# Optimization experiments

Hardware: AMD Instinct MI355X
Metric: run time of the kernel (lower is better)

## Reference

```python
import jax, jax.numpy as jnp
import numpy as np

C = 64   # in_planes
F = 40   # n_freq
T = 512  # n_frame
B = 16


def setup_inputs() -> dict:
    key = jax.random.key(0)
    kx, kq, kk, kv = jax.random.split(key, 4)
    x = jax.random.normal(kx, (B, C, F, T), dtype=jnp.float32)
    # 1x1 conv weights, no bias: [out_ch, in_ch]
    s = 1.0 / np.sqrt(C)
    Wq = jax.random.uniform(kq, (C, C), dtype=jnp.float32, minval=-s, maxval=s)
    Wk = jax.random.uniform(kk, (C, C), dtype=jnp.float32, minval=-s, maxval=s)
    Wv = jax.random.uniform(kv, (C, C), dtype=jnp.float32, minval=-s, maxval=s)
    return {"x": x, "Wq": Wq, "Wk": Wk, "Wv": Wv}


def _proj_tokens(W, x):
    # 1x1 conv (channel mix) then permute(0,3,2,1) + view -> [B, T, F*C]
    y = jnp.einsum('oc,bcft->btfo', W, x)      # [B, T, F, C]
    b, t, f, c = y.shape
    return y.reshape(b, t, f * c)


def reference(x, Wq, Wk, Wv):
    n_batch, n_planes, n_freq, n_frame = x.shape
    d = n_freq * n_planes
    q = _proj_tokens(Wq, x)                     # [B, T, d]
    k = _proj_tokens(Wk, x)
    v = _proj_tokens(Wv, x)
    scores = jnp.einsum('bqd,bkd->bqk', q, k) / jnp.sqrt(jnp.float32(d))
    attn = jax.nn.softmax(scores, axis=-1)      # [B, T, T]
    out = jnp.einsum('bqk,bkd->bqd', attn, v)   # [B, T, d]
    out = out.reshape(n_batch, n_frame, n_freq, n_planes)
    return jnp.transpose(out, (0, 3, 2, 1))     # [B, C, F, T]
```

## Files before the change

kernel.cpp:

```cpp
#include <hip/hip_runtime.h>

constexpr int B_ = 16, C_ = 64, F_ = 40, T_ = 512;
constexpr int D_ = F_ * C_;
constexpr float SCALE = 0.019764235376052372f;

typedef __attribute__((ext_vector_type(8))) short s16x8;
typedef __attribute__((ext_vector_type(4))) short s16x4;
typedef __attribute__((ext_vector_type(4))) float f32x4;

static __device__ __forceinline__ short f2bf(float f) {
  union { float f; unsigned u; } v; v.f = f;
  unsigned r = v.u + 0x7fffu + ((v.u >> 16) & 1u);
  return (short)(r >> 16);
}

static __device__ __forceinline__ f32x4 mfma16(s16x8 a, s16x8 b, f32x4 c) {
  return __builtin_amdgcn_mfma_f32_16x16x32_bf16(a, b, c, 0, 0, 0);
}

static __device__ __forceinline__ void gl2lds16(const short* g, short* l) {
  __builtin_amdgcn_global_load_lds(
      (const __attribute__((address_space(1))) unsigned int*)g,
      (__attribute__((address_space(3))) unsigned int*)l, 16, 0, 0);
}

__global__ __launch_bounds__(256) void wcvt_kernel(
    const float* __restrict__ Wq, const float* __restrict__ Wk,
    const float* __restrict__ Wv, short* __restrict__ Wb)
{
  const int i = blockIdx.x * 256 + threadIdx.x;
  const float* src = (i < 1024) ? Wq : (i < 2048) ? Wk : Wv;
  const float sc = (i < 1024) ? SCALE : 1.0f;
  const float4 v = *(const float4*)(src + (i & 1023) * 4);
  s16x4 s;
  s[0] = f2bf(v.x * sc); s[1] = f2bf(v.y * sc);
  s[2] = f2bf(v.z * sc); s[3] = f2bf(v.w * sc);
  *(s16x4*)&Wb[i * 4] = s;
}

__global__ __launch_bounds__(256) void proj_kernel(
    const float* __restrict__ x, const short* __restrict__ Wb,
    short* __restrict__ Q, short* __restrict__ K, short* __restrict__ V)
{
  constexpr int XS = 132;
  __shared__ __align__(16) short Xl[64 * XS];

  const int b = blockIdx.z, f = blockIdx.y, tt = blockIdx.x;
  const int tid = threadIdx.x;

  const float* xp = x + (((size_t)b * 64) * 40 + f) * 512 + tt * 128;
  #pragma unroll
  for (int it = 0; it < 8; ++it) {
    const int i = tid + it * 256;
    const int c = i >> 5, j = i & 31;
    const float4 v4 = *(const float4*)(xp + (size_t)c * (F_ * T_) + j * 4);
    s16x4 s4; s4[0] = f2bf(v4.x); s4[1] = f2bf(v4.y);
    s4[2] = f2bf(v4.z); s4[3] = f2bf(v4.w);
    *(s16x4*)&Xl[c * XS + j * 4] = s4;
  }
  __syncthreads();

  const int w = tid >> 6, lane = tid & 63;
  const int quad = lane >> 4, c16 = lane & 15;
  const int tl = w * 32;

  s16x8 bfrag[2][2];
  #pragma unroll
  for (int ni = 0; ni < 2; ++ni)
    #pragma unroll
    for (int ks = 0; ks < 2; ++ks) {
      const int t = tl + ni * 16 + c16;
      const int cb = ks * 32 + quad * 8;
      s16x8 tmp;
      #pragma unroll
      for (int j = 0; j < 8; ++j) tmp[j] = Xl[(cb + j) * XS + t];
      bfrag[ni][ks] = tmp;
    }

  #pragma unroll
  for (int p = 0; p < 3; ++p) {
    const short* Wp = Wb + p * 4096;
    s16x8 wfrag[4][2];
    #pragma unroll
    for (int mi = 0; mi < 4; ++mi)
      #pragma unroll
      for (int ks = 0; ks < 2; ++ks)
        wfrag[mi][ks] = *(const s16x8*)(Wp + (mi * 16 + c16) * 64 + ks * 32 + quad * 8);

    if (p < 2) {
      f32x4 acc[4][2] = {};
      #pragma unroll
      for (int ks = 0; ks < 2; ++ks)
        #pragma unroll
        for (int mi = 0; mi < 4; ++mi)
          #pragma unroll
          for (int ni = 0; ni < 2; ++ni)
            acc[mi][ni] = mfma16(wfrag[mi][ks], bfrag[ni][ks], acc[mi][ni]);
      short* outp = (p == 0) ? Q : K;
      #pragma unroll
      for (int mi = 0; mi < 4; ++mi)
        #pragma unroll
        for (int ni = 0; ni < 2; ++ni) {
          const int t = tt * 128 + tl + ni * 16 + c16;
          const int o = mi * 16 + quad * 4;
          s16x4 s4;
          #pragma unroll
          for (int r = 0; r < 4; ++r) s4[r] = f2bf(acc[mi][ni][r]);
          *(s16x4*)&outp[((size_t)(b * 512 + t)) * D_ + f * 64 + o] = s4;
        }
    } else {
      f32x4 acc[2][4] = {};
      #pragma unroll
      for (int ks = 0; ks < 2; ++ks)
        #pragma unroll
        for (int ni = 0; ni < 2; ++ni)
          #pragma unroll
          for (int mi = 0; mi < 4; ++mi)
            acc[ni][mi] = mfma16(bfrag[ni][ks], wfrag[mi][ks], acc[ni][mi]);
      #pragma unroll
      for (int ni = 0; ni < 2; ++ni)
        #pragma unroll
        for (int mi = 0; mi < 4; ++mi) {
          const int t = tt * 128 + tl + ni * 16 + quad * 4;
          const int o = mi * 16 + c16;
          s16x4 s4;
          #pragma unroll
          for (int r = 0; r < 4; ++r) s4[r] = f2bf(acc[ni][mi][r]);
          *(s16x4*)&V[((size_t)(b * D_ + f * 64 + o)) * 512 + t] = s4;
        }
    }
  }
}

__global__ __launch_bounds__(256) void scores_kernel(
    const short* __restrict__ Q, const short* __restrict__ K,
    float* __restrict__ S)
{
  __shared__ __align__(16) short As[64 * 64];
  __shared__ __align__(16) short Bs[128 * 64];
  const int b = blockIdx.y;
  const int mt = blockIdx.x >> 2, nt = blockIdx.x & 3;
  const int m0 = mt * 64, n0 = nt * 128;
  const int tid = threadIdx.x;
  const int w = tid >> 6, lane = tid & 63, quad = lane >> 4, c16 = lane & 15;
  const int wm = (w >> 1) * 32, wn = (w & 1) * 64;

  const short* qb = Q + (size_t)(b * 512 + m0) * D_;
  const short* kb = K + (size_t)(b * 512 + n0) * D_;

  const short* agp[2];
  short* aldsb[2];
  #pragma unroll
  for (int i = 0; i < 2; ++i) {
    const int s = i * 256 + tid, row = s >> 3;
    const int g = (s & 7) ^ (row & 7);
    agp[i] = qb + (size_t)row * D_ + g * 8;
    aldsb[i] = &As[(i * 256 + w * 64) * 8];
  }
  const short* bgp[4];
  short* bldsb[4];
  #pragma unroll
  for (int i = 0; i < 4; ++i) {
    const int s = i * 256 + tid, row = s >> 3;
    const int g = (s & 7) ^ (row & 7);
    bgp[i] = kb + (size_t)row * D_ + g * 8;
    bldsb[i] = &Bs[(i * 256 + w * 64) * 8];
  }

  const short* amp[2][2];
  #pragma unroll
  for (int mi = 0; mi < 2; ++mi)
    #pragma unroll
    for (int ks = 0; ks < 2; ++ks) {
      const int row = wm + mi * 16 + c16;
      const int g = (ks * 4 + quad) ^ (row & 7);
      amp[mi][ks] = &As[row * 64 + g * 8];
    }
  const short* bmp[4][2];
  #pragma unroll
  for (int ni = 0; ni < 4; ++ni)
    #pragma unroll
    for (int ks = 0; ks < 2; ++ks) {
      const int row = wn + ni * 16 + c16;
      const int g = (ks * 4 + quad) ^ (row & 7);
      bmp[ni][ks] = &Bs[row * 64 + g * 8];
    }

  f32x4 acc[2][4] = {};
  constexpr int NK = D_ / 64;
  for (int kk = 0; kk < NK; ++kk) {
    const int ko = kk * 64;
    __syncthreads();
    #pragma unroll
    for (int i = 0; i < 2; ++i) gl2lds16(agp[i] + ko, aldsb[i]);
    #pragma unroll
    for (int i = 0; i < 4; ++i) gl2lds16(bgp[i] + ko, bldsb[i]);
    __syncthreads();
    s16x8 am[2][2], bm[4][2];
    #pragma unroll
    for (int mi = 0; mi < 2; ++mi)
      #pragma unroll
      for (int ks = 0; ks < 2; ++ks) am[mi][ks] = *(const s16x8*)amp[mi][ks];
    #pragma unroll
    for (int ni = 0; ni < 4; ++ni)
      #pragma unroll
      for (int ks = 0; ks < 2; ++ks) bm[ni][ks] = *(const s16x8*)bmp[ni][ks];
    #pragma unroll
    for (int ks = 0; ks < 2; ++ks)
      #pragma unroll
      for (int mi = 0; mi < 2; ++mi)
        #pragma unroll
        for (int ni = 0; ni < 4; ++ni)
          acc[mi][ni] = mfma16(am[mi][ks], bm[ni][ks], acc[mi][ni]);
  }

  float* sp = S + (size_t)b * 512 * 512;
  #pragma unroll
  for (int mi = 0; mi < 2; ++mi)
    #pragma unroll
    for (int ni = 0; ni < 4; ++ni) {
      const int kcol = n0 + wn + ni * 16 + c16;
      const int qr = m0 + wm + mi * 16 + quad * 4;
      #pragma unroll
      for (int r = 0; r < 4; ++r)
        sp[(size_t)(qr + r) * 512 + kcol] = acc[mi][ni][r];
    }
}

__global__ __launch_bounds__(256) void softmax_kernel(
    const float* __restrict__ S, short* __restrict__ A)
{
  const int b = blockIdx.y;
  const int tid = threadIdx.x, w = tid >> 6, lane = tid & 63;
  const int q = blockIdx.x * 4 + w;
  const float* row = S + ((size_t)b * 512 + q) * 512;

  const float4 v0 = *(const float4*)(row + lane * 4);
  const float4 v1 = *(const float4*)(row + 256 + lane * 4);
  float e[8] = {v0.x, v0.y, v0.z, v0.w, v1.x, v1.y, v1.z, v1.w};

  float m = e[0];
  #pragma unroll
  for (int i = 1; i < 8; ++i) m = fmaxf(m, e[i]);
  #pragma unroll
  for (int off = 1; off < 64; off <<= 1) m = fmaxf(m, __shfl_xor(m, off));

  float s = 0.f;
  #pragma unroll
  for (int i = 0; i < 8; ++i) { e[i] = __expf(e[i] - m); s += e[i]; }
  #pragma unroll
  for (int off = 1; off < 64; off <<= 1) s += __shfl_xor(s, off);

  const float inv = 1.0f / s;
  short* arow = A + ((size_t)b * 512 + q) * 512;
  s16x4 o0, o1;
  #pragma unroll
  for (int i = 0; i < 4; ++i) { o0[i] = f2bf(e[i] * inv); o1[i] = f2bf(e[i + 4] * inv); }
  *(s16x4*)&arow[lane * 4] = o0;
  *(s16x4*)&arow[256 + lane * 4] = o1;
}

__global__ __launch_bounds__(256) void pv_kernel(
    const short* __restrict__ A, const short* __restrict__ V,
    float* __restrict__ out)
{
  __shared__ __align__(16) short As[128 * 64];
  __shared__ __align__(16) short Bs[128 * 64];
  const int b = blockIdx.y;
  const int mt = blockIdx.x / 20, dt = blockIdx.x % 20;
  const int m0 = mt * 128, n0 = dt * 128;
  const int tid = threadIdx.x;
  const int w = tid >> 6, lane = tid & 63, quad = lane >> 4, c16 = lane & 15;
  const int wm = (w >> 1) * 64, wn = (w & 1) * 64;

  const short* ab = A + ((size_t)b * 512 + m0) * 512;
  const short* vb = V + ((size_t)b * D_ + n0) * 512;

  const short* agp[4]; short* aldsb[4];
  const short* bgp[4]; short* bldsb[4];
  #pragma unroll
  for (int i = 0; i < 4; ++i) {
    const int s = i * 256 + tid, row = s >> 3;
    const int g = (s & 7) ^ (row & 7);
    agp[i] = ab + (size_t)row * 512 + g * 8;
    bgp[i] = vb + (size_t)row * 512 + g * 8;
    aldsb[i] = &As[(i * 256 + w * 64) * 8];
    bldsb[i] = &Bs[(i * 256 + w * 64) * 8];
  }

  const short* amp[4][2];
  const short* bmp[4][2];
  #pragma unroll
  for (int mi = 0; mi < 4; ++mi)
    #pragma unroll
    for (int ks = 0; ks < 2; ++ks) {
      const int rowa = wm + mi * 16 + c16;
      const int rowb = wn + mi * 16 + c16;
      amp[mi][ks] = &As[rowa * 64 + (((ks * 4 + quad) ^ (rowa & 7)) * 8)];
      bmp[mi][ks] = &Bs[rowb * 64 + (((ks * 4 + quad) ^ (rowb & 7)) * 8)];
    }

  f32x4 acc[4][4] = {};
  constexpr int NK = 512 / 64;
  for (int kk = 0; kk < NK; ++kk) {
    const int ko = kk * 64;
    __syncthreads();
    #pragma unroll
    for (int i = 0; i < 4; ++i) gl2lds16(agp[i] + ko, aldsb[i]);
    #pragma unroll
    for (int i = 0; i < 4; ++i) gl2lds16(bgp[i] + ko, bldsb[i]);
    __syncthreads();
    s16x8 am[4][2], bm[4][2];
    #pragma unroll
    for (int mi = 0; mi < 4; ++mi)
      #pragma unroll
      for (int ks = 0; ks < 2; ++ks) {
        am[mi][ks] = *(const s16x8*)amp[mi][ks];
        bm[mi][ks] = *(const s16x8*)bmp[mi][ks];
      }
    #pragma unroll
    for (int ks = 0; ks < 2; ++ks)
      #pragma unroll
      for (int mi = 0; mi < 4; ++mi)
        #pragma unroll
        for (int ni = 0; ni < 4; ++ni)
          acc[mi][ni] = mfma16(am[mi][ks], bm[ni][ks], acc[mi][ni]);
  }

  #pragma unroll
  for (int mi = 0; mi < 4; ++mi)
    #pragma unroll
    for (int ni = 0; ni < 4; ++ni) {
      const int d = n0 + wn + ni * 16 + c16;
      const int ff = d >> 6, cc = d & 63;
      const int t = m0 + wm + mi * 16 + quad * 4;
      float4 o4;
      o4.x = acc[mi][ni][0]; o4.y = acc[mi][ni][1];
      o4.z = acc[mi][ni][2]; o4.w = acc[mi][ni][3];
      *(float4*)&out[(((size_t)b * 64 + cc) * 40 + ff) * 512 + t] = o4;
    }
}

extern "C" void kernel_launch(void* const* d_in, const int* in_sizes, int n_in,
                              void* d_out, int out_size, void* d_ws, size_t ws_size,
                              hipStream_t stream)
{
  const float* x  = (const float*)d_in[0];
  const float* Wq = (const float*)d_in[1];
  const float* Wk = (const float*)d_in[2];
  const float* Wv = (const float*)d_in[3];
  float* out = (float*)d_out;

  char* ws = (char*)d_ws;
  constexpr size_t QB = (size_t)B_ * T_ * D_ * 2;
  short* Q  = (short*)(ws);
  short* Kt = (short*)(ws + QB);
  short* Vt = (short*)(ws + 2 * QB);
  float* S  = (float*)(ws + 3 * QB);
  short* Wb = (short*)(ws + 3 * QB);
  short* At = (short*)(ws + 3 * QB + (size_t)B_ * T_ * T_ * 4);

  wcvt_kernel<<<dim3(12), 256, 0, stream>>>(Wq, Wk, Wv, Wb);
  proj_kernel<<<dim3(4, 40, 16), 256, 0, stream>>>(x, Wb, Q, Kt, Vt);
  scores_kernel<<<dim3(32, 16), 256, 0, stream>>>(Q, Kt, S);
  softmax_kernel<<<dim3(128, 16), 256, 0, stream>>>(S, At);
  pv_kernel<<<dim3(80, 16), 256, 0, stream>>>(At, Vt, out);
}
```

Before: 274.9 us.

## Double-buffer scores GEMM, pipeline projection tiles, remap grids, use packed bf16 conversion

The scores kernel moves to 128x128 tiles with 512 threads and a double-buffered LDS pipeline. This removes one barrier per k-step and overlaps the next tile's global-to-LDS load with the MFMAs. The projection kernel now handles two time tiles per block, prefetching the second tile into registers while the first is computed. The scores and pv grids are flattened and remapped to group blocks by batch for better L2 locality, and the manual bf16 rounding is replaced with the packed hardware conversion intrinsic. The larger LDS footprint and the extra register pressure from prefetching may lower occupancy.

```diff
diff --git a/kernel.cpp b/kernel.cpp
--- a/kernel.cpp
+++ b/kernel.cpp
@@ -1,4 +1,5 @@
 #include <hip/hip_runtime.h>
+#include <hip/hip_bf16.h>
 
 constexpr int B_ = 16, C_ = 64, F_ = 40, T_ = 512;
 constexpr int D_ = F_ * C_;
@@ -14,6 +15,11 @@
   return (short)(r >> 16);
 }
 
+static __device__ __forceinline__ unsigned int pk2(float a, float b) {
+  __hip_bfloat162 h = __float22bfloat162_rn(make_float2(a, b));
+  union { __hip_bfloat162 h; unsigned int u; } cv; cv.h = h; return cv.u;
+}
+
 static __device__ __forceinline__ f32x4 mfma16(s16x8 a, s16x8 b, f32x4 c) {
   return __builtin_amdgcn_mfma_f32_16x16x32_bf16(a, b, c, 0, 0, 0);
 }
@@ -32,115 +38,133 @@
   const float* src = (i < 1024) ? Wq : (i < 2048) ? Wk : Wv;
   const float sc = (i < 1024) ? SCALE : 1.0f;
   const float4 v = *(const float4*)(src + (i & 1023) * 4);
-  s16x4 s;
-  s[0] = f2bf(v.x * sc); s[1] = f2bf(v.y * sc);
-  s[2] = f2bf(v.z * sc); s[3] = f2bf(v.w * sc);
-  *(s16x4*)&Wb[i * 4] = s;
-}
-
-__global__ __launch_bounds__(256) void proj_kernel(
+  uint2 u; u.x = pk2(v.x * sc, v.y * sc); u.y = pk2(v.z * sc, v.w * sc);
+  *(uint2*)&Wb[i * 4] = u;
+}
+
+__global__ void proj_kernel(
     const float* __restrict__ x, const short* __restrict__ Wb,
     short* __restrict__ Q, short* __restrict__ K, short* __restrict__ V)
 {
   constexpr int XS = 132;
-  __shared__ __align__(16) short Xl[64 * XS];
-
-  const int b = blockIdx.z, f = blockIdx.y, tt = blockIdx.x;
+  __shared__ __align__(16) short Xl[2][64 * XS];
+
+  const int b = blockIdx.z, f = blockIdx.y, th = blockIdx.x;
   const int tid = threadIdx.x;
-
-  const float* xp = x + (((size_t)b * 64) * 40 + f) * 512 + tt * 128;
-  #pragma unroll
-  for (int it = 0; it < 8; ++it) {
-    const int i = tid + it * 256;
-    const int c = i >> 5, j = i & 31;
-    const float4 v4 = *(const float4*)(xp + (size_t)c * (F_ * T_) + j * 4);
-    s16x4 s4; s4[0] = f2bf(v4.x); s4[1] = f2bf(v4.y);
-    s4[2] = f2bf(v4.z); s4[3] = f2bf(v4.w);
-    *(s16x4*)&Xl[c * XS + j * 4] = s4;
-  }
-  __syncthreads();
-
   const int w = tid >> 6, lane = tid & 63;
   const int quad = lane >> 4, c16 = lane & 15;
   const int tl = w * 32;
-
-  s16x8 bfrag[2][2];
-  #pragma unroll
-  for (int ni = 0; ni < 2; ++ni)
-    #pragma unroll
-    for (int ks = 0; ks < 2; ++ks) {
-      const int t = tl + ni * 16 + c16;
-      const int cb = ks * 32 + quad * 8;
-      s16x8 tmp;
-      #pragma unroll
-      for (int j = 0; j < 8; ++j) tmp[j] = Xl[(cb + j) * XS + t];
-      bfrag[ni][ks] = tmp;
-    }
-
-  #pragma unroll
-  for (int p = 0; p < 3; ++p) {
-    const short* Wp = Wb + p * 4096;
-    s16x8 wfrag[4][2];
-    #pragma unroll
-    for (int mi = 0; mi < 4; ++mi)
-      #pragma unroll
-      for (int ks = 0; ks < 2; ++ks)
-        wfrag[mi][ks] = *(const s16x8*)(Wp + (mi * 16 + c16) * 64 + ks * 32 + quad * 8);
-
-    if (p < 2) {
-      f32x4 acc[4][2] = {};
-      #pragma unroll
-      for (int ks = 0; ks < 2; ++ks)
+  const float* xbase = x + (((size_t)b * 64) * 40 + f) * 512;
+
+  auto load_tile = [&](int tt, float4* r) {
+    const float* xp = xbase + tt * 128;
+    #pragma unroll
+    for (int it = 0; it < 8; ++it) {
+      const int i = tid + it * 256;
+      r[it] = *(const float4*)(xp + (size_t)(i >> 5) * (F_ * T_) + (i & 31) * 4);
+    }
+  };
+  auto cvt_store_tile = [&](int buf, const float4* r) {
+    #pragma unroll
+    for (int it = 0; it < 8; ++it) {
+      const int i = tid + it * 256;
+      uint2 u; u.x = pk2(r[it].x, r[it].y); u.y = pk2(r[it].z, r[it].w);
+      *(uint2*)&Xl[buf][(i >> 5) * XS + (i & 31) * 4] = u;
+    }
+  };
+
+  auto process_tile = [&](int buf, int tt) {
+    s16x8 bfrag[2][2];
+    #pragma unroll
+    for (int ni = 0; ni < 2; ++ni)
+      #pragma unroll
+      for (int ks = 0; ks < 2; ++ks) {
+        const int t = tl + ni * 16 + c16;
+        const int cb = ks * 32 + quad * 8;
+        s16x8 tmp;
+        #pragma unroll
+        for (int j = 0; j < 8; ++j) tmp[j] = Xl[buf][(cb + j) * XS + t];
+        bfrag[ni][ks] = tmp;
+      }
+    #pragma unroll
+    for (int p = 0; p < 3; ++p) {
+      const short* Wp = Wb + p * 4096;
+      s16x8 wfrag[4][2];
+      #pragma unroll
+      for (int mi = 0; mi < 4; ++mi)
+        #pragma unroll
+        for (int ks = 0; ks < 2; ++ks)
+          wfrag[mi][ks] = *(const s16x8*)(Wp + (mi * 16 + c16) * 64 + ks * 32 + quad * 8);
+
+      if (p < 2) {
+        f32x4 acc[4][2] = {};
+        #pragma unroll
+        for (int ks = 0; ks < 2; ++ks)
+          #pragma unroll
+          for (int mi = 0; mi < 4; ++mi)
+            #pragma unroll
+            for (int ni = 0; ni < 2; ++ni)
+              acc[mi][ni] = mfma16(wfrag[mi][ks], bfrag[ni][ks], acc[mi][ni]);
+        short* outp = (p == 0) ? Q : K;
         #pragma unroll
         for (int mi = 0; mi < 4; ++mi)
           #pragma unroll
+          for (int ni = 0; ni < 2; ++ni) {
+            const int t = tt * 128 + tl + ni * 16 + c16;
+            const int o = mi * 16 + quad * 4;
+            uint2 u;
+            u.x = pk2(acc[mi][ni][0], acc[mi][ni][1]);
+            u.y = pk2(acc[mi][ni][2], acc[mi][ni][3]);
+            *(uint2*)&outp[((size_t)(b * 512 + t)) * D_ + f * 64 + o] = u;
+          }
+      } else {
+        f32x4 acc[2][4] = {};
+        #pragma unroll
+        for (int ks = 0; ks < 2; ++ks)
+          #pragma unroll
           for (int ni = 0; ni < 2; ++ni)
-            acc[mi][ni] = mfma16(wfrag[mi][ks], bfrag[ni][ks], acc[mi][ni]);
-      short* outp = (p == 0) ? Q : K;
-      #pragma unroll
-      for (int mi = 0; mi < 4; ++mi)
-        #pragma unroll
-        for (int ni = 0; ni < 2; ++ni) {
-          const int t = tt * 128 + tl + ni * 16 + c16;
-          const int o = mi * 16 + quad * 4;
-          s16x4 s4;
-          #pragma unroll
-          for (int r = 0; r < 4; ++r) s4[r] = f2bf(acc[mi][ni][r]);
-          *(s16x4*)&outp[((size_t)(b * 512 + t)) * D_ + f * 64 + o] = s4;
-        }
-    } else {
-      f32x4 acc[2][4] = {};
-      #pragma unroll
-      for (int ks = 0; ks < 2; ++ks)
+            #pragma unroll
+            for (int mi = 0; mi < 4; ++mi)
+              acc[ni][mi] = mfma16(bfrag[ni][ks], wfrag[mi][ks], acc[ni][mi]);
         #pragma unroll
         for (int ni = 0; ni < 2; ++ni)
           #pragma unroll
-          for (int mi = 0; mi < 4; ++mi)
-            acc[ni][mi] = mfma16(bfrag[ni][ks], wfrag[mi][ks], acc[ni][mi]);
-      #pragma unroll
-      for (int ni = 0; ni < 2; ++ni)
-        #pragma unroll
-        for (int mi = 0; mi < 4; ++mi) {
-          const int t = tt * 128 + tl + ni * 16 + quad * 4;
-          const int o = mi * 16 + c16;
-          s16x4 s4;
-          #pragma unroll
-          for (int r = 0; r < 4; ++r) s4[r] = f2bf(acc[ni][mi][r]);
-          *(s16x4*)&V[((size_t)(b * D_ + f * 64 + o)) * 512 + t] = s4;
-        }
-    }
-  }
-}
-
-__global__ __launch_bounds__(256) void scores_kernel(
+          for (int mi = 0; mi < 4; ++mi) {
+            const int t = tt * 128 + tl + ni * 16 + quad * 4;
+            const int o = mi * 16 + c16;
+            uint2 u;
+            u.x = pk2(acc[ni][mi][0], acc[ni][mi][1]);
+            u.y = pk2(acc[ni][mi][2], acc[ni][mi][3]);
+            *(uint2*)&V[((size_t)(b * D_ + f * 64 + o)) * 512 + t] = u;
+          }
+      }
+    }
+  };
+
+  float4 r0[8], r1[8];
+  load_tile(th * 2, r0);
+  cvt_store_tile(0, r0);
+  __syncthreads();
+  load_tile(th * 2 + 1, r1);
+  process_tile(0, th * 2);
+  cvt_store_tile(1, r1);
+  __syncthreads();
+  process_tile(1, th * 2 + 1);
+}
+
+__global__ __launch_bounds__(512) void scores_kernel(
     const short* __restrict__ Q, const short* __restrict__ K,
     float* __restrict__ S)
 {
-  __shared__ __align__(16) short As[64 * 64];
-  __shared__ __align__(16) short Bs[128 * 64];
-  const int b = blockIdx.y;
-  const int mt = blockIdx.x >> 2, nt = blockIdx.x & 3;
-  const int m0 = mt * 64, n0 = nt * 128;
+  __shared__ __align__(16) short As[2][128 * 64];
+  __shared__ __align__(16) short Bs[2][128 * 64];
+
+  const int flat = blockIdx.x;
+  const int rr = flat & 7, qq = flat >> 3;
+  const int nt = qq & 3, p = (qq >> 2) * 8 + rr;
+  const int b = p >> 2, mt = p & 3;
+  const int m0 = mt * 128, n0 = nt * 128;
+
   const int tid = threadIdx.x;
   const int w = tid >> 6, lane = tid & 63, quad = lane >> 4, c16 = lane & 15;
   const int wm = (w >> 1) * 32, wn = (w & 1) * 64;
@@ -148,63 +172,61 @@
   const short* qb = Q + (size_t)(b * 512 + m0) * D_;
   const short* kb = K + (size_t)(b * 512 + n0) * D_;
 
-  const short* agp[2];
-  short* aldsb[2];
+  const short* agp[2]; const short* bgp[2]; int soff[2];
   #pragma unroll
   for (int i = 0; i < 2; ++i) {
-    const int s = i * 256 + tid, row = s >> 3;
+    const int s = i * 512 + tid, row = s >> 3;
     const int g = (s & 7) ^ (row & 7);
     agp[i] = qb + (size_t)row * D_ + g * 8;
-    aldsb[i] = &As[(i * 256 + w * 64) * 8];
-  }
-  const short* bgp[4];
-  short* bldsb[4];
-  #pragma unroll
-  for (int i = 0; i < 4; ++i) {
-    const int s = i * 256 + tid, row = s >> 3;
-    const int g = (s & 7) ^ (row & 7);
     bgp[i] = kb + (size_t)row * D_ + g * 8;
-    bldsb[i] = &Bs[(i * 256 + w * 64) * 8];
-  }
-
-  const short* amp[2][2];
+    soff[i] = (i * 512 + w * 64) * 8;
+  }
+
+  int amoff[2][2], bmoff[4][2];
   #pragma unroll
   for (int mi = 0; mi < 2; ++mi)
     #pragma unroll
     for (int ks = 0; ks < 2; ++ks) {
       const int row = wm + mi * 16 + c16;
-      const int g = (ks * 4 + quad) ^ (row & 7);
-      amp[mi][ks] = &As[row * 64 + g * 8];
-    }
-  const short* bmp[4][2];
+      amoff[mi][ks] = row * 64 + (((ks * 4 + quad) ^ (row & 7)) * 8);
+    }
   #pragma unroll
   for (int ni = 0; ni < 4; ++ni)
     #pragma unroll
     for (int ks = 0; ks < 2; ++ks) {
       const int row = wn + ni * 16 + c16;
-      const int g = (ks * 4 + quad) ^ (row & 7);
-      bmp[ni][ks] = &Bs[row * 64 + g * 8];
+      bmoff[ni][ks] = row * 64 + (((ks * 4 + quad) ^ (row & 7)) * 8);
     }
 
   f32x4 acc[2][4] = {};
   constexpr int NK = D_ / 64;
+
+  #pragma unroll
+  for (int i = 0; i < 2; ++i) {
+    gl2lds16(agp[i], &As[0][soff[i]]);
+    gl2lds16(bgp[i], &Bs[0][soff[i]]);
+  }
+
   for (int kk = 0; kk < NK; ++kk) {
-    const int ko = kk * 64;
+    const int buf = kk & 1;
     __syncthreads();
-    #pragma unroll
-    for (int i = 0; i < 2; ++i) gl2lds16(agp[i] + ko, aldsb[i]);
-    #pragma unroll
-    for (int i = 0; i < 4; ++i) gl2lds16(bgp[i] + ko, bldsb[i]);
-    __syncthreads();
+    if (kk + 1 < NK) {
+      const int ko = (kk + 1) * 64;
+      #pragma unroll
+      for (int i = 0; i < 2; ++i) {
+        gl2lds16(agp[i] + ko, &As[buf ^ 1][soff[i]]);
+        gl2lds16(bgp[i] + ko, &Bs[buf ^ 1][soff[i]]);
+      }
+    }
     s16x8 am[2][2], bm[4][2];
     #pragma unroll
     for (int mi = 0; mi < 2; ++mi)
       #pragma unroll
-      for (int ks = 0; ks < 2; ++ks) am[mi][ks] = *(const s16x8*)amp[mi][ks];
+      for (int ks = 0; ks < 2; ++ks) am[mi][ks] = *(const s16x8*)&As[buf][amoff[mi][ks]];
     #pragma unroll
     for (int ni = 0; ni < 4; ++ni)
       #pragma unroll
-      for (int ks = 0; ks < 2; ++ks) bm[ni][ks] = *(const s16x8*)bmp[ni][ks];
+      for (int ks = 0; ks < 2; ++ks) bm[ni][ks] = *(const s16x8*)&Bs[buf][bmoff[ni][ks]];
     #pragma unroll
     for (int ks = 0; ks < 2; ++ks)
       #pragma unroll
@@ -253,11 +275,11 @@
 
   const float inv = 1.0f / s;
   short* arow = A + ((size_t)b * 512 + q) * 512;
-  s16x4 o0, o1;
-  #pragma unroll
-  for (int i = 0; i < 4; ++i) { o0[i] = f2bf(e[i] * inv); o1[i] = f2bf(e[i + 4] * inv); }
-  *(s16x4*)&arow[lane * 4] = o0;
-  *(s16x4*)&arow[256 + lane * 4] = o1;
+  uint2 o0, o1;
+  o0.x = pk2(e[0] * inv, e[1] * inv); o0.y = pk2(e[2] * inv, e[3] * inv);
+  o1.x = pk2(e[4] * inv, e[5] * inv); o1.y = pk2(e[6] * inv, e[7] * inv);
+  *(uint2*)&arow[lane * 4] = o0;
+  *(uint2*)&arow[256 + lane * 4] = o1;
 }
 
 __global__ __launch_bounds__(256) void pv_kernel(
@@ -266,9 +288,13 @@
 {
   __shared__ __align__(16) short As[128 * 64];
   __shared__ __align__(16) short Bs[128 * 64];
-  const int b = blockIdx.y;
-  const int mt = blockIdx.x / 20, dt = blockIdx.x % 20;
+
+  const int flat = blockIdx.x;
+  const int rr = flat & 7, qq = flat >> 3;
+  const int dt = qq % 20, p = (qq / 20) * 8 + rr;
+  const int b = p >> 2, mt = p & 3;
   const int m0 = mt * 128, n0 = dt * 128;
+
   const int tid = threadIdx.x;
   const int w = tid >> 6, lane = tid & 63, quad = lane >> 4, c16 = lane & 15;
   const int wm = (w >> 1) * 64, wn = (w & 1) * 64;
@@ -361,8 +387,8 @@
   short* At = (short*)(ws + 3 * QB + (size_t)B_ * T_ * T_ * 4);
 
   wcvt_kernel<<<dim3(12), 256, 0, stream>>>(Wq, Wk, Wv, Wb);
-  proj_kernel<<<dim3(4, 40, 16), 256, 0, stream>>>(x, Wb, Q, Kt, Vt);
-  scores_kernel<<<dim3(32, 16), 256, 0, stream>>>(Q, Kt, S);
+  proj_kernel<<<dim3(2, 40, 16), 256, 0, stream>>>(x, Wb, Q, Kt, Vt);
+  scores_kernel<<<dim3(256), 512, 0, stream>>>(Q, Kt, S);
   softmax_kernel<<<dim3(128, 16), 256, 0, stream>>>(S, At);
-  pv_kernel<<<dim3(80, 16), 256, 0, stream>>>(At, Vt, out);
-}
+  pv_kernel<<<dim3(1280), 256, 0, stream>>>(At, Vt, out);
+}
```

New measurement: 300.9 us. +9.5%, slower.
